# Performance work log

Hardware: AMD Instinct MI355X
Metric: run time of the kernel (lower is better)

## Reference

```python
import jax, jax.numpy as jnp
import numpy as np

K = 3  # involution kernel size


def dwconv3x3(x, w, b):
    # x: [B,C,H,W], w: [C,1,3,3] (depthwise, groups=C), b: [C]
    y = jax.lax.conv_general_dilated(
        x, w, window_strides=(1, 1), padding='SAME',
        dimension_numbers=('NCHW', 'OIHW', 'NCHW'),
        feature_group_count=x.shape[1])
    return y + b[None, :, None, None]


def conv1x1(x, w, b):
    # x: [B,C,H,W], w: [O,C], b: [O]
    return jnp.einsum('oc,bchw->bohw', w, x) + b[None, :, None, None]


def extract_patches(x):
    # x: [B,C,H,W] -> [B,C,K*K,H,W], zero-padded 'same' 3x3 neighborhoods
    B, C, H, W = x.shape
    p = (K - 1) // 2
    xp = jnp.pad(x, ((0, 0), (0, 0), (p, p), (p, p)))
    return jnp.stack([xp[:, :, i:i + H, j:j + W]
                      for i in range(K) for j in range(K)], axis=2)


def involution(x, w_red, b_red, w_span, b_span):
    # dynamic per-pixel kernels: [B, K*K, H, W]
    kern = conv1x1(jax.nn.relu(conv1x1(x, w_red, b_red)), w_span, b_span)
    patches = extract_patches(x)                 # [B,C,KK,H,W]
    return jnp.einsum('bkhw,bckhw->bchw', kern, patches)


def setup_inputs() -> dict:
    key = jax.random.key(0)
    ks = jax.random.split(key, 10)
    dim, red = 256, 64  # reduction ratio 4
    B, H, W = 8, 64, 64
    s = 0.05
    return {
        'x': jax.random.normal(ks[0], (B, dim, H, W), jnp.float32),
        'w_in': jax.random.normal(ks[1], (dim, 1, 3, 3), jnp.float32) * s,
        'b_in': jax.random.normal(ks[2], (dim,), jnp.float32) * s,
        'w_red': jax.random.normal(ks[3], (red, dim), jnp.float32) * s,
        'b_red': jax.random.normal(ks[4], (red,), jnp.float32) * s,
        'w_span': jax.random.normal(ks[5], (K * K, red), jnp.float32) * s,
        'b_span': jax.random.normal(ks[6], (K * K,), jnp.float32) * s,
        'w_out': jax.random.normal(ks[7], (dim, 1, 3, 3), jnp.float32) * s,
        'b_out': jax.random.normal(ks[8], (dim,), jnp.float32) * s,
    }


def reference(x, w_in, b_in, w_red, b_red, w_span, b_span, w_out, b_out):
    x = dwconv3x3(x, w_in, b_in)
    x = involution(x, w_red, b_red, w_span, b_span)
    x = dwconv3x3(x, w_out, b_out)
    return x
```

## Files before the change

### kernel.cpp

```cpp
#include <hip/hip_runtime.h>

#define BB 8
#define CC 256
#define HH 64
#define WW 64
#define RED 64
#define HW 4096
#define LS 68

__global__ __launch_bounds__(256) void dwconv1(const float* __restrict__ x,
                                               const float* __restrict__ w,
                                               const float* __restrict__ bias,
                                               float* __restrict__ out,
                                               const float* __restrict__ w_red,
                                               float* __restrict__ wt) {
    const int t = threadIdx.x;
    const int c = blockIdx.y, b = blockIdx.z;
    if (blockIdx.x == 4) {
        if (b == 0 && t < RED) wt[c * RED + t] = w_red[t * CC + c];
        return;
    }
    const int q  = t & 15;
    const int w0 = q << 2;
    const int h  = (blockIdx.x << 4) + (t >> 4);
    const float* xp = x + ((size_t)(b * CC + c)) * HW;
    const float* wp = w + c * 9;
    const float bb = bias[c];
    float4 acc = make_float4(bb, bb, bb, bb);
    #pragma unroll
    for (int ky = 0; ky < 3; ky++) {
        int hh = h + ky - 1;
        if (hh < 0 || hh >= HH) continue;
        const float* row = xp + hh * WW + w0;
        float4 v = *(const float4*)row;
        float lf = (w0 > 0)      ? row[-1] : 0.f;
        float rt = (w0 + 4 < WW) ? row[4]  : 0.f;
        float k0 = wp[ky * 3 + 0], k1 = wp[ky * 3 + 1], k2 = wp[ky * 3 + 2];
        acc.x = fmaf(k0, lf,  acc.x); acc.y = fmaf(k0, v.x, acc.y);
        acc.z = fmaf(k0, v.y, acc.z); acc.w = fmaf(k0, v.z, acc.w);
        acc.x = fmaf(k1, v.x, acc.x); acc.y = fmaf(k1, v.y, acc.y);
        acc.z = fmaf(k1, v.z, acc.z); acc.w = fmaf(k1, v.w, acc.w);
        acc.x = fmaf(k2, v.y, acc.x); acc.y = fmaf(k2, v.z, acc.y);
        acc.z = fmaf(k2, v.w, acc.z); acc.w = fmaf(k2, rt,  acc.w);
    }
    *(float4*)(out + ((size_t)(b * CC + c)) * HW + h * WW + w0) = acc;
}

__global__ __launch_bounds__(512) void kern_gen(const float* __restrict__ x1,
                                                const float* __restrict__ wt,
                                                const float* __restrict__ b_red,
                                                const float* __restrict__ w_span,
                                                const float* __restrict__ b_span,
                                                float* __restrict__ kern) {
    __shared__ float xs[64 * 64];
    __shared__ float part[8 * 9 * 64];
    const int t  = threadIdx.x;
    const int px = t & 63;
    const int og = t >> 6;
    const int o0 = __builtin_amdgcn_readfirstlane(og << 3);
    const int pixel0 = blockIdx.x * 64;
    const int b   = pixel0 >> 12;
    const int hw0 = pixel0 & 4095;
    const float* xbase = x1 + (size_t)b * CC * HW + hw0;

    float acc[8];
    #pragma unroll
    for (int i = 0; i < 8; i++) acc[i] = 0.f;

    for (int c0 = 0; c0 < CC; c0 += 64) {
        #pragma unroll
        for (int k = 0; k < 8; k++) {
            int i  = t + k * 512;
            int cc = i >> 6, pp = i & 63;
            xs[i] = xbase[(size_t)(c0 + cc) * HW + pp];
        }
        __syncthreads();
        const float* wrow = wt + c0 * RED + o0;
        #pragma unroll 8
        for (int c = 0; c < 64; c++) {
            float xv = xs[c * 64 + px];
            #pragma unroll
            for (int i = 0; i < 8; i++) acc[i] = fmaf(wrow[c * RED + i], xv, acc[i]);
        }
        __syncthreads();
    }

    float kk[9];
    #pragma unroll
    for (int j = 0; j < 9; j++) kk[j] = 0.f;
    #pragma unroll
    for (int i = 0; i < 8; i++) {
        float r = fmaxf(acc[i] + b_red[o0 + i], 0.f);
        #pragma unroll
        for (int j = 0; j < 9; j++) kk[j] = fmaf(w_span[j * RED + o0 + i], r, kk[j]);
    }

    #pragma unroll
    for (int j = 0; j < 9; j++) part[(og * 9 + j) * 64 + px] = kk[j];
    __syncthreads();

    if (og == 0) {
        float* kp = kern + (size_t)b * 9 * HW + hw0 + px;
        #pragma unroll
        for (int j = 0; j < 9; j++) {
            float s = b_span[j];
            #pragma unroll
            for (int g = 0; g < 8; g++) s += part[(g * 9 + j) * 64 + px];
            kp[j * HW] = s;
        }
    }
}

__global__ __launch_bounds__(256) void invol_dw(const float* __restrict__ x1,
                                                const float* __restrict__ kern,
                                                const float* __restrict__ w_out,
                                                const float* __restrict__ b_out,
                                                float* __restrict__ out) {
    __shared__ float xs[HH * LS];
    __shared__ float ys[HH * LS];
    const int t  = threadIdx.x;
    const int q  = t & 15;
    const int w0 = q << 2;
    const int r  = t >> 4;
    const int c = blockIdx.x, b = blockIdx.y;
    const float* xp = x1 + ((size_t)(b * CC + c)) * HW;

    #pragma unroll
    for (int i = 0; i < 4; i++) {
        int h = r + (i << 4);
        *(float4*)&xs[h * LS + w0] = *(const float4*)(xp + h * WW + w0);
    }
    __syncthreads();

    const float* kp = kern + (size_t)b * 9 * HW;
    #pragma unroll
    for (int i = 0; i < 4; i++) {
        int h  = r + (i << 4);
        int hw = h * WW + w0;
        float4 acc = make_float4(0.f, 0.f, 0.f, 0.f);
        #pragma unroll
        for (int ky = 0; ky < 3; ky++) {
            int hh = h + ky - 1;
            if (hh < 0 || hh >= HH) continue;
            const float* row = &xs[hh * LS + w0];
            float4 v = *(const float4*)row;
            float lf = (w0 > 0)      ? row[-1] : 0.f;
            float rt = (w0 + 4 < WW) ? row[4]  : 0.f;
            float4 k0 = *(const float4*)(kp + (ky * 3 + 0) * HW + hw);
            float4 k1 = *(const float4*)(kp + (ky * 3 + 1) * HW + hw);
            float4 k2 = *(const float4*)(kp + (ky * 3 + 2) * HW + hw);
            acc.x = fmaf(k0.x, lf,  acc.x); acc.y = fmaf(k0.y, v.x, acc.y);
            acc.z = fmaf(k0.z, v.y, acc.z); acc.w = fmaf(k0.w, v.z, acc.w);
            acc.x = fmaf(k1.x, v.x, acc.x); acc.y = fmaf(k1.y, v.y, acc.y);
            acc.z = fmaf(k1.z, v.z, acc.z); acc.w = fmaf(k1.w, v.w, acc.w);
            acc.x = fmaf(k2.x, v.y, acc.x); acc.y = fmaf(k2.y, v.z, acc.y);
            acc.z = fmaf(k2.z, v.w, acc.z); acc.w = fmaf(k2.w, rt,  acc.w);
        }
        *(float4*)&ys[h * LS + w0] = acc;
    }
    __syncthreads();

    const float* wp = w_out + c * 9;
    const float bb = b_out[c];
    float* op = out + ((size_t)(b * CC + c)) * HW;
    #pragma unroll
    for (int i = 0; i < 4; i++) {
        int h = r + (i << 4);
        float4 acc = make_float4(bb, bb, bb, bb);
        #pragma unroll
        for (int ky = 0; ky < 3; ky++) {
            int hh = h + ky - 1;
            if (hh < 0 || hh >= HH) continue;
            const float* row = &ys[hh * LS + w0];
            float4 v = *(const float4*)row;
            float lf = (w0 > 0)      ? row[-1] : 0.f;
            float rt = (w0 + 4 < WW) ? row[4]  : 0.f;
            float k0 = wp[ky * 3 + 0], k1 = wp[ky * 3 + 1], k2 = wp[ky * 3 + 2];
            acc.x = fmaf(k0, lf,  acc.x); acc.y = fmaf(k0, v.x, acc.y);
            acc.z = fmaf(k0, v.y, acc.z); acc.w = fmaf(k0, v.z, acc.w);
            acc.x = fmaf(k1, v.x, acc.x); acc.y = fmaf(k1, v.y, acc.y);
            acc.z = fmaf(k1, v.z, acc.z); acc.w = fmaf(k1, v.w, acc.w);
            acc.x = fmaf(k2, v.y, acc.x); acc.y = fmaf(k2, v.z, acc.y);
            acc.z = fmaf(k2, v.w, acc.z); acc.w = fmaf(k2, rt,  acc.w);
        }
        *(float4*)(op + h * WW + w0) = acc;
    }
}

extern "C" void kernel_launch(void* const* d_in, const int* in_sizes, int n_in,
                              void* d_out, int out_size, void* d_ws, size_t ws_size,
                              hipStream_t stream) {
    const float* x      = (const float*)d_in[0];
    const float* w_in   = (const float*)d_in[1];
    const float* b_in   = (const float*)d_in[2];
    const float* w_red  = (const float*)d_in[3];
    const float* b_red  = (const float*)d_in[4];
    const float* w_span = (const float*)d_in[5];
    const float* b_span = (const float*)d_in[6];
    const float* w_out  = (const float*)d_in[7];
    const float* b_out  = (const float*)d_in[8];
    float* out = (float*)d_out;

    float* ws   = (float*)d_ws;
    float* x1   = ws;
    float* kern = x1 + (size_t)BB * CC * HW;
    float* wt   = kern + (size_t)BB * 9 * HW;

    dwconv1<<<dim3(5, CC, BB), 256, 0, stream>>>(x, w_in, b_in, x1, w_red, wt);
    kern_gen<<<512, 512, 0, stream>>>(x1, wt, b_red, w_span, b_span, kern);
    invol_dw<<<dim3(CC, BB), 256, 0, stream>>>(x1, kern, w_out, b_out, out);
}
```

Measured before the change: 153.2 us.

## Fuse first depthwise conv into kernel-generation kernel, drop weight transpose

Merges the first depthwise 3x3 convolution into the kernel-generation kernel. Each block computes one image row for all channels, writes the result to LDS for the reduction GEMV and also to global x1 for the later involution kernel. This removes one launch and the global re-read of x1 by kern_gen. The transposed w_red buffer is dropped, so weights are now read with a strided CC pattern, which may be less cache friendly. Each block also reads three input rows per channel, so halo rows are loaded redundantly across blocks.

```diff
diff --git a/kernel.cpp b/kernel.cpp
--- a/kernel.cpp
+++ b/kernel.cpp
@@ -6,62 +6,29 @@
 #define WW 64
 #define RED 64
 #define HW 4096
+#define XS 68
 #define LS 68
 
-__global__ __launch_bounds__(256) void dwconv1(const float* __restrict__ x,
-                                               const float* __restrict__ w,
-                                               const float* __restrict__ bias,
-                                               float* __restrict__ out,
+__global__ __launch_bounds__(512) void dw_kern(const float* __restrict__ x,
+                                               const float* __restrict__ w_in,
+                                               const float* __restrict__ b_in,
                                                const float* __restrict__ w_red,
-                                               float* __restrict__ wt) {
-    const int t = threadIdx.x;
-    const int c = blockIdx.y, b = blockIdx.z;
-    if (blockIdx.x == 4) {
-        if (b == 0 && t < RED) wt[c * RED + t] = w_red[t * CC + c];
-        return;
-    }
-    const int q  = t & 15;
-    const int w0 = q << 2;
-    const int h  = (blockIdx.x << 4) + (t >> 4);
-    const float* xp = x + ((size_t)(b * CC + c)) * HW;
-    const float* wp = w + c * 9;
-    const float bb = bias[c];
-    float4 acc = make_float4(bb, bb, bb, bb);
-    #pragma unroll
-    for (int ky = 0; ky < 3; ky++) {
-        int hh = h + ky - 1;
-        if (hh < 0 || hh >= HH) continue;
-        const float* row = xp + hh * WW + w0;
-        float4 v = *(const float4*)row;
-        float lf = (w0 > 0)      ? row[-1] : 0.f;
-        float rt = (w0 + 4 < WW) ? row[4]  : 0.f;
-        float k0 = wp[ky * 3 + 0], k1 = wp[ky * 3 + 1], k2 = wp[ky * 3 + 2];
-        acc.x = fmaf(k0, lf,  acc.x); acc.y = fmaf(k0, v.x, acc.y);
-        acc.z = fmaf(k0, v.y, acc.z); acc.w = fmaf(k0, v.z, acc.w);
-        acc.x = fmaf(k1, v.x, acc.x); acc.y = fmaf(k1, v.y, acc.y);
-        acc.z = fmaf(k1, v.z, acc.z); acc.w = fmaf(k1, v.w, acc.w);
-        acc.x = fmaf(k2, v.y, acc.x); acc.y = fmaf(k2, v.z, acc.y);
-        acc.z = fmaf(k2, v.w, acc.z); acc.w = fmaf(k2, rt,  acc.w);
-    }
-    *(float4*)(out + ((size_t)(b * CC + c)) * HW + h * WW + w0) = acc;
-}
-
-__global__ __launch_bounds__(512) void kern_gen(const float* __restrict__ x1,
-                                                const float* __restrict__ wt,
-                                                const float* __restrict__ b_red,
-                                                const float* __restrict__ w_span,
-                                                const float* __restrict__ b_span,
-                                                float* __restrict__ kern) {
-    __shared__ float xs[64 * 64];
+                                               const float* __restrict__ b_red,
+                                               const float* __restrict__ w_span,
+                                               const float* __restrict__ b_span,
+                                               float* __restrict__ x1,
+                                               float* __restrict__ kern) {
+    __shared__ float xs[64 * XS];
     __shared__ float part[8 * 9 * 64];
     const int t  = threadIdx.x;
+    const int h  = blockIdx.x;
+    const int b  = blockIdx.y;
     const int px = t & 63;
     const int og = t >> 6;
     const int o0 = __builtin_amdgcn_readfirstlane(og << 3);
-    const int pixel0 = blockIdx.x * 64;
-    const int b   = pixel0 >> 12;
-    const int hw0 = pixel0 & 4095;
-    const float* xbase = x1 + (size_t)b * CC * HW + hw0;
+    const int q  = t & 15;
+    const int w0 = q << 2;
+    const int cr = t >> 4;
 
     float acc[8];
     #pragma unroll
@@ -69,18 +36,40 @@
 
     for (int c0 = 0; c0 < CC; c0 += 64) {
         #pragma unroll
-        for (int k = 0; k < 8; k++) {
-            int i  = t + k * 512;
-            int cc = i >> 6, pp = i & 63;
-            xs[i] = xbase[(size_t)(c0 + cc) * HW + pp];
+        for (int s = 0; s < 2; s++) {
+            const int cl = s * 32 + cr;
+            const int cc = c0 + cl;
+            const float* xp = x + ((size_t)(b * CC + cc)) * HW;
+            const float* wp = w_in + cc * 9;
+            const float bb = b_in[cc];
+            float4 a4 = make_float4(bb, bb, bb, bb);
+            #pragma unroll
+            for (int ky = 0; ky < 3; ky++) {
+                int hh = h + ky - 1;
+                if (hh < 0 || hh >= HH) continue;
+                const float* row = xp + hh * WW + w0;
+                float4 v = *(const float4*)row;
+                float lf = (w0 > 0)      ? row[-1] : 0.f;
+                float rt = (w0 + 4 < WW) ? row[4]  : 0.f;
+                float k0 = wp[ky * 3 + 0], k1 = wp[ky * 3 + 1], k2 = wp[ky * 3 + 2];
+                a4.x = fmaf(k0, lf,  a4.x); a4.y = fmaf(k0, v.x, a4.y);
+                a4.z = fmaf(k0, v.y, a4.z); a4.w = fmaf(k0, v.z, a4.w);
+                a4.x = fmaf(k1, v.x, a4.x); a4.y = fmaf(k1, v.y, a4.y);
+                a4.z = fmaf(k1, v.z, a4.z); a4.w = fmaf(k1, v.w, a4.w);
+                a4.x = fmaf(k2, v.y, a4.x); a4.y = fmaf(k2, v.z, a4.y);
+                a4.z = fmaf(k2, v.w, a4.z); a4.w = fmaf(k2, rt,  a4.w);
+            }
+            *(float4*)&xs[cl * XS + w0] = a4;
+            *(float4*)(x1 + ((size_t)(b * CC + cc)) * HW + h * WW + w0) = a4;
         }
         __syncthreads();
-        const float* wrow = wt + c0 * RED + o0;
+        const float* wr = w_red + o0 * CC + c0;
         #pragma unroll 8
         for (int c = 0; c < 64; c++) {
-            float xv = xs[c * 64 + px];
+            float xv = xs[c * XS + px];
             #pragma unroll
-            for (int i = 0; i < 8; i++) acc[i] = fmaf(wrow[c * RED + i], xv, acc[i]);
+            for (int i = 0; i < 8; i++)
+                acc[i] = fmaf(wr[i * CC + c], xv, acc[i]);
         }
         __syncthreads();
     }
@@ -94,13 +83,11 @@
         #pragma unroll
         for (int j = 0; j < 9; j++) kk[j] = fmaf(w_span[j * RED + o0 + i], r, kk[j]);
     }
-
     #pragma unroll
     for (int j = 0; j < 9; j++) part[(og * 9 + j) * 64 + px] = kk[j];
     __syncthreads();
-
     if (og == 0) {
-        float* kp = kern + (size_t)b * 9 * HW + hw0 + px;
+        float* kp = kern + (size_t)b * 9 * HW + h * WW + px;
         #pragma unroll
         for (int j = 0; j < 9; j++) {
             float s = b_span[j];
@@ -204,9 +191,8 @@
     float* ws   = (float*)d_ws;
     float* x1   = ws;
     float* kern = x1 + (size_t)BB * CC * HW;
-    float* wt   = kern + (size_t)BB * 9 * HW;
 
-    dwconv1<<<dim3(5, CC, BB), 256, 0, stream>>>(x, w_in, b_in, x1, w_red, wt);
-    kern_gen<<<512, 512, 0, stream>>>(x1, wt, b_red, w_span, b_span, kern);
+    dw_kern<<<dim3(HH, BB), 512, 0, stream>>>(x, w_in, b_in, w_red, b_red,
+                                              w_span, b_span, x1, kern);
     invol_dw<<<dim3(CC, BB), 256, 0, stream>>>(x1, kern, w_out, b_out, out);
 }
```

After: 151.8 us. Within noise of the previous version (-0.9%).
